# Kernel tuning notes

Hardware: AMD Instinct MI355X
Metric: run time of the kernel (lower is better)

The kernel has to match this reference:

```python
import jax, jax.numpy as jnp
import numpy as np
from jax import lax

N = 8192  # total_nodes


def setup_inputs() -> dict:
    key = jax.random.key(0)
    kx, kW = jax.random.split(key)
    x = jax.random.normal(kx, (2,), dtype=jnp.float32)
    W = jax.random.normal(kW, (N, N), dtype=jnp.float32) * 0.1
    b = jnp.zeros((N,), dtype=jnp.float32)
    return {"x": x, "W": W, "b": b}


def reference(x, W, b):
    # Sequential DAG scan: s[j] = sigmoid(sum_{i<j} W[i,j] * s[i] + b[j])
    # (triu mask with diagonal=1 is all-ones over the slice [:j, j])
    n = W.shape[0]
    idx = jnp.arange(n)
    s0 = jnp.zeros((n,), dtype=W.dtype).at[0].set(x[0]).at[1].set(x[1])

    def step(s, j):
        m = (idx < j).astype(s.dtype)          # strict-upper-triangular mask column
        ws = jnp.sum(W[:, j] * m * s)          # weighted sum over predecessors
        val = jax.nn.sigmoid(ws + b[j])
        return s.at[j].set(val), None

    s, _ = lax.scan(step, s0, jnp.arange(2, n))
    return s[n - 1]
```

## Files before the change

### kernel.cpp

```cpp
#include <hip/hip_runtime.h>

#define NN 8192
#define SBS 512
#define NSB 16
#define LOG2E 1.44269504088896f

#define FR(k,w) (32 + ((k)*8 + (w))*32)
#define PART_OFF 8192
#define CP_OFF   16384
#define NCPROW   9
#define SARR_OFF (CP_OFF + NCPROW * NN)

__device__ __forceinline__ float bcastf(float v, int lane) {
    return __int_as_float(__builtin_amdgcn_readlane(__float_as_int(v), lane));
}
__device__ __forceinline__ float sigm(float prelog) {
    return __builtin_amdgcn_rcpf(1.0f + __builtin_amdgcn_exp2f(-prelog));
}
__device__ __forceinline__ int ld_flag(const int* p) {
    return __hip_atomic_load(p, __ATOMIC_RELAXED, __HIP_MEMORY_SCOPE_AGENT);
}
__device__ __forceinline__ void st_rel(int* p, int v) {
    __hip_atomic_store(p, v, __ATOMIC_RELEASE, __HIP_MEMORY_SCOPE_AGENT);
}
__device__ __forceinline__ float ldf(const float* p) {
    return __hip_atomic_load(p, __ATOMIC_RELAXED, __HIP_MEMORY_SCOPE_AGENT);
}
__device__ __forceinline__ void stf(float* p, float v) {
    __hip_atomic_store(p, v, __ATOMIC_RELAXED, __HIP_MEMORY_SCOPE_AGENT);
}
#define LBAR() do { asm volatile("s_waitcnt lgkmcnt(0)\ns_barrier" ::: "memory"); \
                    __builtin_amdgcn_sched_barrier(0); } while (0)

__global__ void init_ws(int* wsi, float* wsf) {
    int i = blockIdx.x * 256 + threadIdx.x;
    if (i < 8192) wsi[i] = 0;
    wsf[CP_OFF + i] = 0.0f;
}

__device__ void solver_fn(const float* __restrict__ W, const float* __restrict__ b,
                          const float* __restrict__ x, float* wsf, int* flags,
                          float* sdiag, float* spub, float* sacc,
                          float (*redN)[8][64], float* __restrict__ out, int k) {
    const int tid = threadIdx.x;
    const int w = tid >> 6, l = tid & 63;
    const int dj = tid >> 3, dc = (tid & 7) * 8;
    const int J0 = k * SBS;
    const float* cp = wsf + CP_OFF;
    float* partials = wsf + PART_OFF;
    float* s_arr = wsf + SARR_OFF;

    auto load_diag = [&](int mm, float4& a, float4& bq) {
        if (dj < dc + 7) {
            const float* p = &W[(size_t)(J0 + mm*64 + dj) * NN + (J0 + mm*64 + dc)];
            a  = *(const float4*)p;
            bq = *(const float4*)(p + 4);
        } else {
            a = make_float4(0.f,0.f,0.f,0.f); bq = make_float4(0.f,0.f,0.f,0.f);
        }
    };
    auto write_diag = [&](int mm, float4 a, float4 bq) {
        float* dst = &sdiag[mm*4096 + dj*64 + dc];
        float v[8] = {a.x, a.y, a.z, a.w, bq.x, bq.y, bq.z, bq.w};
        #pragma unroll
        for (int e = 0; e < 8; ++e) dst[e] = (dj < dc + e) ? v[e] * LOG2E : 0.0f;
    };
    auto load_pan1 = [&](int mm, float* pr) {
        #pragma unroll
        for (int r = 0; r < 8; ++r)
            pr[r] = W[(size_t)(J0 + mm*64 + w*8 + r) * NN + (J0 + (mm+1)*64 + l)];
    };

    const float x0 = x[0], x1 = x[1];
    float base = b[J0 + tid];
    #pragma unroll
    for (int r = 0; r < NCPROW; ++r) base += cp[r * NN + J0 + tid];
    float4 dA[2], dB[2];
    load_diag(0, dA[0], dB[0]);
    load_diag(1, dA[1], dB[1]);
    float p1[2][8];
    load_pan1(0, p1[0]);
    load_pan1(1, p1[1]);
    write_diag(0, dA[0], dB[0]);
    write_diag(1, dA[1], dB[1]);
    sacc[tid] = base;
    LBAR();

    #pragma unroll
    for (int m = 0; m < 8; ++m) {
        if (w == m) {
            float part = 0.0f;
            if (m >= 2) {
                const int* fl = &flags[FR(k, m)];
                while (ld_flag(fl) == 0) {}
                __builtin_amdgcn_fence(__ATOMIC_ACQUIRE, "agent");
                part = ldf(&partials[((size_t)k*8 + m)*64 + l]);
            }
            float rsum = 0.0f;
            if (m >= 1) {
                #pragma unroll
                for (int g = 0; g < 8; ++g) rsum += redN[m & 1][g][l];
            }
            float acc = (sacc[m*64 + l] + rsum + part) * LOG2E;
            float smine = 0.0f;
            const bool first = (k == 0) && (m == 0);
            #pragma unroll
            for (int j = 0; j < 64; ++j) {
                const float pre = bcastf(acc, j);
                float s;
                if (first && j == 0)      s = x0;
                else if (first && j == 1) s = x1;
                else                      s = sigm(pre);
                acc += sdiag[m*4096 + j*64 + l] * s;
                if (l == j) smine = s;
            }
            spub[m*64 + l] = smine;
            stf(&s_arr[J0 + m*64 + l], smine);
            if (k == NSB - 1 && m == 7 && l == 63) out[0] = smine;
            if (l == 0) st_rel(&flags[0], k*8 + m + 1);
        }
        LBAR();
        if (m < 7) {
            float f1 = 0.0f;
            #pragma unroll
            for (int r = 0; r < 8; ++r)
                f1 += p1[m & 1][r] * spub[m*64 + w*8 + r];
            redN[(m+1) & 1][w][l] = f1;
            if (m >= 1) write_diag(m + 1, dA[(m+1) & 1], dB[(m+1) & 1]);
            if (m + 2 <= 7) load_diag(m + 2, dA[(m+2) & 1], dB[(m+2) & 1]);
            if (m + 2 <= 6) load_pan1(m + 2, p1[m & 1]);
            LBAR();
        }
    }
}

template <int TW>
__device__ void helper_fn(const float* __restrict__ W, float* wsf, int* flags,
                          float (*redh)[64], int k) {
    const int tid = threadIdx.x, g = tid >> 6, l = tid & 63;
    float* partials = wsf + PART_OFF;
    const float* s_arr = wsf + SARR_OFF;
    const int J0 = k * SBS;

    float pr[TW - 1][8];
    #pragma unroll
    for (int m = 0; m <= TW - 2; ++m)
        #pragma unroll
        for (int r = 0; r < 8; ++r)
            pr[m][r] = W[(size_t)(J0 + m*64 + g*8 + r) * NN + (J0 + TW*64 + l)];

    float part = 0.0f;
    #pragma unroll
    for (int m = 0; m <= TW - 2; ++m) {
        if (tid < 64) {
            while (ld_flag(&flags[0]) < k*8 + m + 1) __builtin_amdgcn_s_sleep(1);
        }
        __syncthreads();
        __builtin_amdgcn_fence(__ATOMIC_ACQUIRE, "agent");
        #pragma unroll
        for (int r = 0; r < 8; ++r)
            part += pr[m][r] * ldf(&s_arr[J0 + m*64 + g*8 + r]);
    }
    redh[g][l] = part;
    __syncthreads();
    if (tid < 64) {
        float tot = 0.0f;
        #pragma unroll
        for (int g2 = 0; g2 < 8; ++g2) tot += redh[g2][tid];
        stf(&partials[((size_t)k*8 + TW)*64 + tid], tot);
    }
    __syncthreads();
    if (tid == 0) st_rel(&flags[FR(k, TW)], 1);
}

__device__ void prefetch_fn(const float* __restrict__ W, int k) {
    const int tid = threadIdx.x;
    const int w = tid >> 6, l = tid & 63;
    const int dj = tid >> 3, dc = (tid & 7) * 8;
    const int J0 = (k + 1) * SBS;
    float s = 0.0f;
    #pragma unroll
    for (int mm = 0; mm < 8; ++mm) {
        if (dj < dc + 7) {
            const float* p = &W[(size_t)(J0 + mm*64 + dj) * NN + (J0 + mm*64 + dc)];
            float4 a = *(const float4*)p, bq = *(const float4*)(p + 4);
            s += (a.x + a.y) + (a.z + a.w) + (bq.x + bq.y) + (bq.z + bq.w);
        }
    }
    #pragma unroll
    for (int mm = 0; mm < 7; ++mm)
        #pragma unroll
        for (int r = 0; r < 8; ++r)
            s += W[(size_t)(J0 + mm*64 + w*8 + r) * NN + (J0 + (mm+1)*64 + l)];
    asm volatile("" :: "v"(s));
}

__device__ void near_fn(const float* __restrict__ W, float* wsf, int* flags,
                        float (*redh)[64], int t, int k) {
    const int tid = threadIdx.x, g = tid >> 6, l = tid & 63;
    const int col = (k+1)*SBS + t*64 + l;
    const float* s_arr = wsf + SARR_OFF;
    float* cp = wsf + CP_OFF;

    float pr[8][8];
    #pragma unroll
    for (int m = 0; m < 8; ++m)
        #pragma unroll
        for (int r = 0; r < 8; ++r)
            pr[m][r] = W[(size_t)(k*SBS + m*64 + g*8 + r) * NN + col];

    float part = 0.0f;
    #pragma unroll
    for (int m = 0; m < 8; ++m) {
        if (tid < 64) {
            while (ld_flag(&flags[0]) < k*8 + m + 1) __builtin_amdgcn_s_sleep(4);
        }
        __syncthreads();
        __builtin_amdgcn_fence(__ATOMIC_ACQUIRE, "agent");
        #pragma unroll
        for (int r = 0; r < 8; ++r)
            part += pr[m][r] * ldf(&s_arr[k*SBS + m*64 + g*8 + r]);
    }
    redh[g][l] = part;
    __syncthreads();
    if (g == 0) {
        float tot = 0.0f;
        #pragma unroll
        for (int g2 = 0; g2 < 8; ++g2) tot += redh[g2][l];
        cp[8 * NN + col] = tot;
    }
}

__device__ void bulk_fn(const float* __restrict__ W, float* wsf,
                        float* ssh, int idx, int k) {
    const int tid = threadIdx.x;
    const int rc = idx & 7, cg = idx >> 3;
    const int row0 = (k-1)*SBS + rc*64;
    const int col = (k+1)*SBS + cg*SBS + tid;
    const float* s_arr = wsf + SARR_OFF;
    float* cp = wsf + CP_OFF;

    if (tid < 64) ssh[tid] = s_arr[row0 + tid];
    __syncthreads();
    const float* wp = W + (size_t)row0 * NN + col;
    float a0 = 0.f, a1 = 0.f, a2 = 0.f, a3 = 0.f;
    #pragma unroll
    for (int i = 0; i < 64; i += 4) {
        a0 += wp[(size_t)(i + 0) * NN] * ssh[i + 0];
        a1 += wp[(size_t)(i + 1) * NN] * ssh[i + 1];
        a2 += wp[(size_t)(i + 2) * NN] * ssh[i + 2];
        a3 += wp[(size_t)(i + 3) * NN] * ssh[i + 3];
    }
    cp[rc * NN + col] += (a0 + a1) + (a2 + a3);
}

__global__ void __launch_bounds__(512, 1) mega_kernel(
    const float* __restrict__ W, const float* __restrict__ b,
    const float* __restrict__ x, float* wsf, int* flags,
    float* __restrict__ out, int k)
{
    __shared__ float sdiag[8 * 4096];
    __shared__ float spub[512];
    __shared__ float sacc[512];
    __shared__ float redN[2][8][64];
    __shared__ float redh[8][64];
    const int bid = blockIdx.x;
    if (bid == 0) {
        solver_fn(W, b, x, wsf, flags, sdiag, spub, sacc, redN, out, k);
        return;
    }
    if ((bid & 7) == 0 && bid <= 48) {
        switch (bid >> 3) {
            case 1: helper_fn<2>(W, wsf, flags, redh, k); break;
            case 2: helper_fn<3>(W, wsf, flags, redh, k); break;
            case 3: helper_fn<4>(W, wsf, flags, redh, k); break;
            case 4: helper_fn<5>(W, wsf, flags, redh, k); break;
            case 5: helper_fn<6>(W, wsf, flags, redh, k); break;
            case 6: helper_fn<7>(W, wsf, flags, redh, k); break;
        }
        return;
    }
    if (bid == 56) {
        if (k < NSB - 1) prefetch_fn(W, k);
        return;
    }
    if (bid < 10) {
        if (k < NSB - 1) near_fn(W, wsf, flags, redh, (bid < 8) ? bid - 1 : 7, k);
        return;
    }
    if (k >= 1) {
        int nh = (bid >> 3) - 1; if (nh > 6) nh = 6;
        int idx = bid - 10 - nh;
        if (idx < 8 * (15 - k)) bulk_fn(W, wsf, &redh[0][0], idx, k);
    }
}

extern "C" void kernel_launch(void* const* d_in, const int* in_sizes, int n_in,
                              void* d_out, int out_size, void* d_ws, size_t ws_size,
                              hipStream_t stream) {
    const float* x = (const float*)d_in[0];
    const float* W = (const float*)d_in[1];
    const float* b = (const float*)d_in[2];
    float* out = (float*)d_out;
    float* wsf = (float*)d_ws;
    int* wsi   = (int*)d_ws;

    init_ws<<<dim3(288), dim3(256), 0, stream>>>(wsi, wsf);
    for (int k = 0; k < NSB; ++k) {
        int nb;
        if (k == 0)            nb = 57;
        else if (k == NSB - 1) nb = 49;
        else if (k <= 9)       nb = 8 * (15 - k) + 16;
        else                   nb = 57;
        mega_kernel<<<dim3(nb), dim3(512), 0, stream>>>(W, b, x, wsf, wsi, out, k);
    }
}
```

Measured before the change: 449.0 us.

## Restructure solver pipeline: per-wave 64-row panel, deferred s publishing, simplified block roles

The solver now has each wave preload a full 64-row panel for the previous 64-block and compute its own cross-block contribution directly from shared memory, replacing the per-step redN reduction and its extra barrier. Publishing of s values and flags is deferred to another wave so it is off the critical wave's path. The last row block of the previous super-block moves into helper/near work. The prefetch block is removed and the block-to-role mapping is simplified, with a matching launch grid. This cuts barriers and sequential latency on the critical path, at the cost of heavier register pressure (64 floats per thread) and changed flag-timing dependencies.

```diff
diff --git a/kernel.cpp b/kernel.cpp
--- a/kernel.cpp
+++ b/kernel.cpp
@@ -40,8 +40,7 @@
 
 __device__ void solver_fn(const float* __restrict__ W, const float* __restrict__ b,
                           const float* __restrict__ x, float* wsf, int* flags,
-                          float* sdiag, float* spub, float* sacc,
-                          float (*redN)[8][64], float* __restrict__ out, int k) {
+                          float* sdiag, float* spub, float* __restrict__ out, int k) {
     const int tid = threadIdx.x;
     const int w = tid >> 6, l = tid & 63;
     const int dj = tid >> 3, dc = (tid & 7) * 8;
@@ -65,43 +64,43 @@
         #pragma unroll
         for (int e = 0; e < 8; ++e) dst[e] = (dj < dc + e) ? v[e] * LOG2E : 0.0f;
     };
-    auto load_pan1 = [&](int mm, float* pr) {
-        #pragma unroll
-        for (int r = 0; r < 8; ++r)
-            pr[r] = W[(size_t)(J0 + mm*64 + w*8 + r) * NN + (J0 + (mm+1)*64 + l)];
-    };
 
     const float x0 = x[0], x1 = x[1];
     float base = b[J0 + tid];
     #pragma unroll
     for (int r = 0; r < NCPROW; ++r) base += cp[r * NN + J0 + tid];
+
+    float p1[64];
+    const int srow = J0 + ((w == 0) ? -64 : (w - 1) * 64);
+    if (k > 0 || w > 0) {
+        #pragma unroll
+        for (int r = 0; r < 64; ++r)
+            p1[r] = W[(size_t)(srow + r) * NN + (J0 + w*64 + l)];
+    }
     float4 dA[2], dB[2];
     load_diag(0, dA[0], dB[0]);
     load_diag(1, dA[1], dB[1]);
-    float p1[2][8];
-    load_pan1(0, p1[0]);
-    load_pan1(1, p1[1]);
+    if (k > 0 && w == 0) spub[512 + l] = s_arr[J0 - 64 + l];
     write_diag(0, dA[0], dB[0]);
-    write_diag(1, dA[1], dB[1]);
-    sacc[tid] = base;
+    float part_w = 0.0f;
     LBAR();
 
     #pragma unroll
     for (int m = 0; m < 8; ++m) {
         if (w == m) {
-            float part = 0.0f;
-            if (m >= 2) {
-                const int* fl = &flags[FR(k, m)];
-                while (ld_flag(fl) == 0) {}
-                __builtin_amdgcn_fence(__ATOMIC_ACQUIRE, "agent");
-                part = ldf(&partials[((size_t)k*8 + m)*64 + l]);
-            }
             float rsum = 0.0f;
-            if (m >= 1) {
+            if (m > 0 || k > 0) {
+                const int soff = (m == 0) ? 512 : (m - 1) * 64;
                 #pragma unroll
-                for (int g = 0; g < 8; ++g) rsum += redN[m & 1][g][l];
-            }
-            float acc = (sacc[m*64 + l] + rsum + part) * LOG2E;
+                for (int r4 = 0; r4 < 16; ++r4) {
+                    float4 sv = *(const float4*)&spub[soff + r4*4];
+                    rsum += p1[r4*4+0]*sv.x + p1[r4*4+1]*sv.y
+                          + p1[r4*4+2]*sv.z + p1[r4*4+3]*sv.w;
+                }
+            }
+            if (m < 7)      write_diag(m + 1, dA[(m+1) & 1], dB[(m+1) & 1]);
+            if (m + 2 <= 7) load_diag(m + 2, dA[(m+2) & 1], dB[(m+2) & 1]);
+            float acc = (base + rsum + part_w) * LOG2E;
             float smine = 0.0f;
             const bool first = (k == 0) && (m == 0);
             #pragma unroll
@@ -115,22 +114,25 @@
                 if (l == j) smine = s;
             }
             spub[m*64 + l] = smine;
-            stf(&s_arr[J0 + m*64 + l], smine);
+            if (m == 7) stf(&s_arr[J0 + 448 + l], smine);
             if (k == NSB - 1 && m == 7 && l == 63) out[0] = smine;
-            if (l == 0) st_rel(&flags[0], k*8 + m + 1);
+        } else {
+            if (w == m + 1 && (w >= 2 || (w == 1 && k > 0))) {
+                const int* fl = &flags[FR(k, w)];
+                while (ld_flag(fl) == 0) {}
+                __builtin_amdgcn_fence(__ATOMIC_ACQUIRE, "agent");
+                part_w = ldf(&partials[((size_t)k*8 + w)*64 + l]);
+            }
+            if (m >= 1 && w == ((m + 3) & 7)) {
+                float val = spub[(m-1)*64 + l];
+                stf(&s_arr[J0 + (m-1)*64 + l], val);
+                if (l == 0) st_rel(&flags[0], k*8 + m);
+                __builtin_amdgcn_sched_barrier(0);
+            }
+            if (m < 7)      write_diag(m + 1, dA[(m+1) & 1], dB[(m+1) & 1]);
+            if (m + 2 <= 7) load_diag(m + 2, dA[(m+2) & 1], dB[(m+2) & 1]);
         }
         LBAR();
-        if (m < 7) {
-            float f1 = 0.0f;
-            #pragma unroll
-            for (int r = 0; r < 8; ++r)
-                f1 += p1[m & 1][r] * spub[m*64 + w*8 + r];
-            redN[(m+1) & 1][w][l] = f1;
-            if (m >= 1) write_diag(m + 1, dA[(m+1) & 1], dB[(m+1) & 1]);
-            if (m + 2 <= 7) load_diag(m + 2, dA[(m+2) & 1], dB[(m+2) & 1]);
-            if (m + 2 <= 6) load_pan1(m + 2, p1[m & 1]);
-            LBAR();
-        }
     }
 }
 
@@ -141,25 +143,37 @@
     float* partials = wsf + PART_OFF;
     const float* s_arr = wsf + SARR_OFF;
     const int J0 = k * SBS;
-
-    float pr[TW - 1][8];
-    #pragma unroll
-    for (int m = 0; m <= TW - 2; ++m)
-        #pragma unroll
-        for (int r = 0; r < 8; ++r)
-            pr[m][r] = W[(size_t)(J0 + m*64 + g*8 + r) * NN + (J0 + TW*64 + l)];
-
+    const int col = J0 + TW*64 + l;
     float part = 0.0f;
-    #pragma unroll
-    for (int m = 0; m <= TW - 2; ++m) {
-        if (tid < 64) {
-            while (ld_flag(&flags[0]) < k*8 + m + 1) __builtin_amdgcn_s_sleep(1);
-        }
-        __syncthreads();
-        __builtin_amdgcn_fence(__ATOMIC_ACQUIRE, "agent");
-        #pragma unroll
-        for (int r = 0; r < 8; ++r)
-            part += pr[m][r] * ldf(&s_arr[J0 + m*64 + g*8 + r]);
+
+    if (k > 0) {
+        float wv[8], sv[8];
+        #pragma unroll
+        for (int r = 0; r < 8; ++r) {
+            wv[r] = W[(size_t)(J0 - 64 + g*8 + r) * NN + col];
+            sv[r] = s_arr[J0 - 64 + g*8 + r];
+        }
+        #pragma unroll
+        for (int r = 0; r < 8; ++r) part += wv[r] * sv[r];
+    }
+    if constexpr (TW >= 2) {
+        float pr[TW - 1][8];
+        #pragma unroll
+        for (int m = 0; m <= TW - 2; ++m)
+            #pragma unroll
+            for (int r = 0; r < 8; ++r)
+                pr[m][r] = W[(size_t)(J0 + m*64 + g*8 + r) * NN + col];
+        #pragma unroll
+        for (int m = 0; m <= TW - 2; ++m) {
+            if (tid < 64) {
+                while (ld_flag(&flags[0]) < k*8 + m + 1) __builtin_amdgcn_s_sleep(1);
+            }
+            __syncthreads();
+            __builtin_amdgcn_fence(__ATOMIC_ACQUIRE, "agent");
+            #pragma unroll
+            for (int r = 0; r < 8; ++r)
+                part += pr[m][r] * ldf(&s_arr[J0 + m*64 + g*8 + r]);
+        }
     }
     redh[g][l] = part;
     __syncthreads();
@@ -171,28 +185,6 @@
     }
     __syncthreads();
     if (tid == 0) st_rel(&flags[FR(k, TW)], 1);
-}
-
-__device__ void prefetch_fn(const float* __restrict__ W, int k) {
-    const int tid = threadIdx.x;
-    const int w = tid >> 6, l = tid & 63;
-    const int dj = tid >> 3, dc = (tid & 7) * 8;
-    const int J0 = (k + 1) * SBS;
-    float s = 0.0f;
-    #pragma unroll
-    for (int mm = 0; mm < 8; ++mm) {
-        if (dj < dc + 7) {
-            const float* p = &W[(size_t)(J0 + mm*64 + dj) * NN + (J0 + mm*64 + dc)];
-            float4 a = *(const float4*)p, bq = *(const float4*)(p + 4);
-            s += (a.x + a.y) + (a.z + a.w) + (bq.x + bq.y) + (bq.z + bq.w);
-        }
-    }
-    #pragma unroll
-    for (int mm = 0; mm < 7; ++mm)
-        #pragma unroll
-        for (int r = 0; r < 8; ++r)
-            s += W[(size_t)(J0 + mm*64 + w*8 + r) * NN + (J0 + (mm+1)*64 + l)];
-    asm volatile("" :: "v"(s));
 }
 
 __device__ void near_fn(const float* __restrict__ W, float* wsf, int* flags,
@@ -202,16 +194,16 @@
     const float* s_arr = wsf + SARR_OFF;
     float* cp = wsf + CP_OFF;
 
-    float pr[8][8];
-    #pragma unroll
-    for (int m = 0; m < 8; ++m)
+    float pr[7][8];
+    #pragma unroll
+    for (int m = 0; m < 7; ++m)
         #pragma unroll
         for (int r = 0; r < 8; ++r)
             pr[m][r] = W[(size_t)(k*SBS + m*64 + g*8 + r) * NN + col];
 
     float part = 0.0f;
     #pragma unroll
-    for (int m = 0; m < 8; ++m) {
+    for (int m = 0; m < 7; ++m) {
         if (tid < 64) {
             while (ld_flag(&flags[0]) < k*8 + m + 1) __builtin_amdgcn_s_sleep(4);
         }
@@ -260,38 +252,25 @@
     float* __restrict__ out, int k)
 {
     __shared__ float sdiag[8 * 4096];
-    __shared__ float spub[512];
-    __shared__ float sacc[512];
-    __shared__ float redN[2][8][64];
+    __shared__ float spub[576];
     __shared__ float redh[8][64];
     const int bid = blockIdx.x;
     if (bid == 0) {
-        solver_fn(W, b, x, wsf, flags, sdiag, spub, sacc, redN, out, k);
-        return;
-    }
-    if ((bid & 7) == 0 && bid <= 48) {
-        switch (bid >> 3) {
-            case 1: helper_fn<2>(W, wsf, flags, redh, k); break;
-            case 2: helper_fn<3>(W, wsf, flags, redh, k); break;
-            case 3: helper_fn<4>(W, wsf, flags, redh, k); break;
-            case 4: helper_fn<5>(W, wsf, flags, redh, k); break;
-            case 5: helper_fn<6>(W, wsf, flags, redh, k); break;
-            case 6: helper_fn<7>(W, wsf, flags, redh, k); break;
-        }
-        return;
-    }
-    if (bid == 56) {
-        if (k < NSB - 1) prefetch_fn(W, k);
-        return;
-    }
-    if (bid < 10) {
-        if (k < NSB - 1) near_fn(W, wsf, flags, redh, (bid < 8) ? bid - 1 : 7, k);
-        return;
-    }
-    if (k >= 1) {
-        int nh = (bid >> 3) - 1; if (nh > 6) nh = 6;
-        int idx = bid - 10 - nh;
-        if (idx < 8 * (15 - k)) bulk_fn(W, wsf, &redh[0][0], idx, k);
+        solver_fn(W, b, x, wsf, flags, sdiag, spub, out, k);
+    } else if (bid <= 7) {
+        switch (bid) {
+            case 1: helper_fn<1>(W, wsf, flags, redh, k); break;
+            case 2: helper_fn<2>(W, wsf, flags, redh, k); break;
+            case 3: helper_fn<3>(W, wsf, flags, redh, k); break;
+            case 4: helper_fn<4>(W, wsf, flags, redh, k); break;
+            case 5: helper_fn<5>(W, wsf, flags, redh, k); break;
+            case 6: helper_fn<6>(W, wsf, flags, redh, k); break;
+            case 7: helper_fn<7>(W, wsf, flags, redh, k); break;
+        }
+    } else if (bid <= 15) {
+        near_fn(W, wsf, flags, redh, bid - 8, k);
+    } else {
+        bulk_fn(W, wsf, &redh[0][0], bid - 16, k);
     }
 }
 
@@ -308,10 +287,9 @@
     init_ws<<<dim3(288), dim3(256), 0, stream>>>(wsi, wsf);
     for (int k = 0; k < NSB; ++k) {
         int nb;
-        if (k == 0)            nb = 57;
-        else if (k == NSB - 1) nb = 49;
-        else if (k <= 9)       nb = 8 * (15 - k) + 16;
-        else                   nb = 57;
+        if (k == 0)            nb = 16;
+        else if (k == NSB - 1) nb = 8;
+        else                   nb = 16 + 8 * (15 - k);
         mega_kernel<<<dim3(nb), dim3(512), 0, stream>>>(W, b, x, wsf, wsi, out, k);
     }
 }
```

Result: slower. 470.0 us (+4.7%).
